# Optimization experiments

Hardware: AMD Instinct MI355X
Metric: run time of the kernel (lower is better)

## Reference

```python
import jax, jax.numpy as jnp
import numpy as np

N, P, D, C = 2048, 64, 512, 32   # bs*n_vars, patch_num, hidden_dim, cluster_num
H, DFF, L = 8, 2048, 3           # heads, ffn dim, encoder layers
TEMP = 10.0
EPS = 1e-10
LN_EPS = 1e-5


def setup_inputs() -> dict:
    key = jax.random.key(0)
    ks = jax.random.split(key, 18)
    s = 0.02  # small init to keep activations sane
    inp = {}
    inp["input_series"] = jax.random.normal(ks[0], (N, P, D), jnp.float32)
    pi = jax.random.uniform(ks[1], (C,), jnp.float32) + 0.1
    inp["text_pi"] = pi / pi.sum()
    A = jax.random.uniform(ks[2], (C, C), jnp.float32) + 0.1
    inp["text_A"] = A / A.sum(axis=1, keepdims=True)
    # stacked per-layer TransformerEncoderLayer params (torch post-norm, relu)
    inp["qkv_w"] = jax.random.normal(ks[3], (L, 3 * D, D), jnp.float32) * s
    inp["qkv_b"] = jnp.zeros((L, 3 * D), jnp.float32)
    inp["out_w"] = jax.random.normal(ks[4], (L, D, D), jnp.float32) * s
    inp["out_b"] = jnp.zeros((L, D), jnp.float32)
    inp["ln1_w"] = jnp.ones((L, D), jnp.float32)
    inp["ln1_b"] = jnp.zeros((L, D), jnp.float32)
    inp["ff1_w"] = jax.random.normal(ks[5], (L, DFF, D), jnp.float32) * s
    inp["ff1_b"] = jnp.zeros((L, DFF), jnp.float32)
    inp["ff2_w"] = jax.random.normal(ks[6], (L, D, DFF), jnp.float32) * s
    inp["ff2_b"] = jnp.zeros((L, D), jnp.float32)
    inp["ln2_w"] = jnp.ones((L, D), jnp.float32)
    inp["ln2_b"] = jnp.zeros((L, D), jnp.float32)
    inp["mus"] = jax.random.normal(ks[7], (C, D), jnp.float32)
    return inp


def _layer_norm(x, w, b):
    m = x.mean(axis=-1, keepdims=True)
    v = ((x - m) ** 2).mean(axis=-1, keepdims=True)
    return (x - m) * jax.lax.rsqrt(v + LN_EPS) * w + b


def _encoder_layer(x, qkv_w, qkv_b, out_w, out_b, ln1_w, ln1_b,
                   ff1_w, ff1_b, ff2_w, ff2_b, ln2_w, ln2_b):
    n, p, d = x.shape
    dh = d // H
    qkv = x @ qkv_w.T + qkv_b                       # [n,p,3d]
    q, k, v = jnp.split(qkv, 3, axis=-1)
    def split_heads(t):
        return t.reshape(n, p, H, dh).transpose(0, 2, 1, 3)  # [n,h,p,dh]
    q, k, v = split_heads(q), split_heads(k), split_heads(v)
    scores = jnp.einsum('nhqd,nhkd->nhqk', q, k) / (dh ** 0.5)
    attn = jax.nn.softmax(scores, axis=-1)
    o = jnp.einsum('nhqk,nhkd->nhqd', attn, v)
    o = o.transpose(0, 2, 1, 3).reshape(n, p, d)
    o = o @ out_w.T + out_b
    x = _layer_norm(x + o, ln1_w, ln1_b)            # post-norm
    f = jax.nn.relu(x @ ff1_w.T + ff1_b) @ ff2_w.T + ff2_b
    return _layer_norm(x + f, ln2_w, ln2_b)


def reference(input_series, text_pi, text_A, qkv_w, qkv_b, out_w, out_b,
              ln1_w, ln1_b, ff1_w, ff1_b, ff2_w, ff2_b, ln2_w, ln2_b, mus):
    x = input_series
    for l in range(L):
        x = _encoder_layer(x, qkv_w[l], qkv_b[l], out_w[l], out_b[l],
                           ln1_w[l], ln1_b[l], ff1_w[l], ff1_b[l],
                           ff2_w[l], ff2_b[l], ln2_w[l], ln2_b[l])
    emb_ts = x                                       # [N,P,D]
    # ClusterCenters: softmax of exp(-||x - tanh(mu)||^2 / T)
    mu = jnp.tanh(mus)                               # [C,D]
    dist = ((emb_ts ** 2).sum(-1)[..., None]
            + (mu ** 2).sum(-1)[None, None, :]
            - 2.0 * jnp.einsum('npd,cd->npc', emb_ts, mu))  # [N,P,C]
    z = jnp.exp(-dist / TEMP)
    logits_all = z / z.sum(axis=-1, keepdims=True)
    log_za = jnp.log(logits_all + EPS)               # [N,P,C]
    # sequential HMM-style recursion over patches
    l0 = jax.nn.softmax(jnp.log(text_pi + EPS)[None, :] + log_za[:, 0], axis=-1)
    def step(c, lz):
        c2 = jax.nn.softmax(jnp.log(c @ text_A + EPS) + lz, axis=-1)
        return c2, c2
    _, ys = jax.lax.scan(step, l0, jnp.swapaxes(log_za[:, 1:], 0, 1))  # [P-1,N,C]
    cluster_probs = jnp.concatenate([l0[:, None], jnp.swapaxes(ys, 0, 1)], axis=1)
    entropy_loss = -jnp.sum(cluster_probs * jnp.log(cluster_probs + EPS), axis=-1).mean()
    return (cluster_probs, emb_ts, text_pi, text_A, entropy_loss)
```

## Files before the change

kernel.cpp:

```cpp
#include <hip/hip_runtime.h>
#include <stdint.h>


typedef __bf16 bf16;
typedef __bf16 bf16x2 __attribute__((ext_vector_type(2)));
typedef __bf16 bf16x4 __attribute__((ext_vector_type(4)));
typedef __bf16 bf16x8 __attribute__((ext_vector_type(8)));
typedef float  f32x4  __attribute__((ext_vector_type(4)));
typedef float  f32x2  __attribute__((ext_vector_type(2)));

#define EPSF 1e-10f
#define NROWS 131072L

__device__ __forceinline__ float bflo(uint32_t u){ return __uint_as_float(u << 16); }
__device__ __forceinline__ float bfhi(uint32_t u){ return __uint_as_float(u & 0xffff0000u); }

__device__ __forceinline__ void gload_lds16(const bf16* g, bf16* l){
  __builtin_amdgcn_global_load_lds((const __attribute__((address_space(1))) uint32_t*)g,
                                   (__attribute__((address_space(3))) uint32_t*)l,
                                   16, 0, 0);
}

__global__ void k_f2bf(const float* __restrict__ in, bf16* __restrict__ out, long n){
  const long stride = (long)gridDim.x * blockDim.x * 4;
  for (long i = ((long)blockIdx.x * blockDim.x + threadIdx.x) * 4; i < n; i += stride){
    f32x4 v = *(const f32x4*)(in + i);
    bf16x4 o = { (bf16)v[0], (bf16)v[1], (bf16)v[2], (bf16)v[3] };
    *(bf16x4*)(out + i) = o;
  }
}


#define MFMA_PH(SM, SN)                                                       \
  {                                                                           \
    __builtin_amdgcn_s_setprio(1);                                            \
    _Pragma("unroll")                                                         \
    for (int kk = 0; kk < 2; kk++) {                                          \
      _Pragma("unroll")                                                       \
      for (int i2 = 0; i2 < 4; i2++) {                                        \
        _Pragma("unroll")                                                     \
        for (int j2 = 0; j2 < 2; j2++) {                                      \
          acc[(SM)*4+i2][(SN)*2+j2] = __builtin_amdgcn_mfma_f32_16x16x32_bf16(\
              a[i2][kk], b[SN][j2][kk], acc[(SM)*4+i2][(SN)*2+j2], 0, 0, 0);  \
        }                                                                     \
      }                                                                       \
    }                                                                         \
    __builtin_amdgcn_s_setprio(0);                                            \
  }

#define RD_A(SM)                                                              \
  _Pragma("unroll")                                                           \
  for (int i2 = 0; i2 < 4; i2++) {                                            \
    a[i2][0] = *(const bf16x8*)&Ac[(SM)*8192 + aBase + i2*1024 + sl0];        \
    a[i2][1] = *(const bf16x8*)&Ac[(SM)*8192 + aBase + i2*1024 + sl1];        \
  }

#define RD_B(SN)                                                              \
  _Pragma("unroll")                                                           \
  for (int j2 = 0; j2 < 2; j2++) {                                            \
    b[SN][j2][0] = *(const bf16x8*)&Bc[(SN)*8192 + bBase + j2*1024 + sl0];    \
    b[SN][j2][1] = *(const bf16x8*)&Bc[(SN)*8192 + bBase + j2*1024 + sl1];    \
  }

#define ISSUE_A(dst, RO, KK) \
  gload_lds16(gA + (long)(RO)*lda + (KK), (dst) + (RO)*64 + wsl)
#define ISSUE_B(dst, RO, KK) \
  gload_lds16(gB + (long)(RO)*K   + (KK), (dst) + (RO)*64 + wsl)

#define WAITV(N)  asm volatile("s_waitcnt vmcnt(" #N ")" ::: "memory")
#define WAITL0    asm volatile("s_waitcnt lgkmcnt(0)" ::: "memory")
#define BARRIER   { __builtin_amdgcn_s_barrier(); asm volatile("" ::: "memory"); }

template<int RELU>
__global__ __launch_bounds__(512, 2)
void gemm256(const bf16* __restrict__ A, long lda,
             const bf16* __restrict__ W,
             const float* __restrict__ bias,
             bf16* __restrict__ Cb, long K, int nbx)
{
  const int tid  = threadIdx.x;
  const int wid  = tid >> 6;
  const int lane = tid & 63;
  const int wr = wid >> 2, wc = wid & 3;
  const long ldc = (long)nbx * 256;

  const unsigned nwg = gridDim.x;
  const unsigned q   = nwg >> 3;
  const unsigned swz = (blockIdx.x & 7) * q + (blockIdx.x >> 3);
  const unsigned bx  = swz % (unsigned)nbx;
  const unsigned by  = swz / (unsigned)nbx;
  const long bm = (long)by * 256;
  const long bn = (long)bx * 256;

  __shared__ __align__(16) bf16 smem[65536];
  bf16* const As0 = smem;
  bf16* const Bs0 = smem + 16384;
  bf16* const As1 = smem + 32768;
  bf16* const Bs1 = smem + 49152;

  const int gswz = ((lane & 7) ^ ((lane >> 3) & 7)) * 8;
  const int wsl  = wid * 512;
  const bf16* gA = A + (bm + wid * 8 + (lane >> 3)) * lda + gswz;
  const bf16* gB = W + (bn + wid * 8 + (lane >> 3)) * K   + gswz;

  const int fr = lane & 15, fg = lane >> 4;
  const int aBase = (wr * 64 + fr) * 64;
  const int bBase = (wc * 32 + fr) * 64;
  const int sl0 = ((0 + fg) ^ (fr & 7)) * 8;
  const int sl1 = ((4 + fg) ^ (fr & 7)) * 8;

  f32x4 acc[8][4];
#pragma unroll
  for (int i = 0; i < 8; i++)
#pragma unroll
    for (int j = 0; j < 4; j++) acc[i][j] = (f32x4){0.f, 0.f, 0.f, 0.f};

  bf16x8 a[4][2];
  bf16x8 b[2][2][2];

  const int nt = (int)(K >> 6);

  ISSUE_A(As0, 0, 0);   ISSUE_A(As0, 64, 0);
  ISSUE_B(Bs0, 0, 0);   ISSUE_B(Bs0, 64, 0);
  ISSUE_A(As0, 128, 0); ISSUE_A(As0, 192, 0);
  ISSUE_B(Bs0, 128, 0); ISSUE_B(Bs0, 192, 0);
  ISSUE_A(As1, 0, 64);  ISSUE_A(As1, 64, 64);
  ISSUE_B(Bs1, 0, 64);  ISSUE_B(Bs1, 64, 64);
  WAITV(4);
  BARRIER;

  for (int t = 0; t < nt; t++){
    bf16* const Ac = (t & 1) ? As1 : As0;
    bf16* const Bc = (t & 1) ? Bs1 : Bs0;
    bf16* const An = (t & 1) ? As0 : As1;
    bf16* const Bn = (t & 1) ? Bs0 : Bs1;
    const bool s1 = (t + 1 < nt);
    const bool s2 = (t + 2 < nt);
    const long kn  = (long)(t + 1) << 6;
    const long kn2 = (long)(t + 2) << 6;

    RD_A(0); RD_B(0); RD_B(1);
    if (s1){ ISSUE_A(An, 128, kn); ISSUE_A(An, 192, kn); }
    WAITL0;
    MFMA_PH(0, 0);
    BARRIER;

    if (s1){ ISSUE_B(Bn, 128, kn); ISSUE_B(Bn, 192, kn); }
    MFMA_PH(0, 1);
    __builtin_amdgcn_sched_barrier(0);
    RD_A(1);
    BARRIER;

    if (s2){ ISSUE_A(Ac, 0, kn2); ISSUE_A(Ac, 64, kn2); }
    WAITL0;
    MFMA_PH(1, 0);
    BARRIER;

    if (s2){ ISSUE_B(Bc, 0, kn2); ISSUE_B(Bc, 64, kn2); }
    MFMA_PH(1, 1);
    if (s2){ WAITV(4); } else { WAITV(0); }
    BARRIER;
  }

  bf16* const cw = smem + wid * 1280;
  float bv[4];
#pragma unroll
  for (int sn = 0; sn < 2; sn++)
#pragma unroll
    for (int j2 = 0; j2 < 2; j2++)
      bv[sn * 2 + j2] = bias[bn + sn * 128 + wc * 32 + j2 * 16 + fr];

#pragma unroll
  for (int sm = 0; sm < 2; sm++){
#pragma unroll
    for (int sn = 0; sn < 2; sn++){
#pragma unroll
      for (int ch = 0; ch < 2; ch++){
#pragma unroll
        for (int i2 = 0; i2 < 2; i2++){
#pragma unroll
          for (int j2 = 0; j2 < 2; j2++){
#pragma unroll
            for (int r = 0; r < 4; r++){
              float v = acc[sm * 4 + ch * 2 + i2][sn * 2 + j2][r] + bv[sn * 2 + j2];
              if (RELU) v = fmaxf(v, 0.f);
              cw[(i2 * 16 + fg * 4 + r) * 40 + j2 * 16 + fr] = (bf16)v;
            }
          }
        }
        WAITL0;
        const long r0 = bm + sm * 128 + wr * 64 + ch * 32;
        const long c0 = bn + sn * 128 + wc * 32;
#pragma unroll
        for (int p = 0; p < 2; p++){
          const int row = p * 16 + (lane >> 2);
          const int colg = (lane & 3) * 8;
          bf16x8 o = *(const bf16x8*)&cw[row * 40 + colg];
          *(bf16x8*)&Cb[(r0 + row) * ldc + c0 + colg] = o;
        }
        WAITL0;
      }
    }
  }
}

__global__ __launch_bounds__(256)
void attention(bf16* __restrict__ qkv)
{
  const int blk = blockIdx.x;
  const long n = blk >> 3;
  const int h  = blk & 7;
  const int tid = threadIdx.x;
  const int wid = tid >> 6, lane = tid & 63;

  __shared__ __align__(16) bf16 Qs[64][72];
  __shared__ __align__(16) bf16 Ks[64][72];
  __shared__ __align__(16) bf16 Vt[64][72];

  bf16* base = qkv + n * 64 * 1536 + h * 64;

  for (int c = tid; c < 512; c += 256){
    const int row = c >> 3, col = (c & 7) * 8;
    const long go = (long)row * 1536 + col;
    *(bf16x8*)&Qs[row][col] = *(const bf16x8*)(base + go);
    *(bf16x8*)&Ks[row][col] = *(const bf16x8*)(base + 512 + go);
    bf16x8 v = *(const bf16x8*)(base + 1024 + go);
#pragma unroll
    for (int e = 0; e < 8; e++) Vt[col + e][row] = v[e];
  }
  __syncthreads();

  const int fr = lane & 15, fg = lane >> 4;
  f32x4 sacc[4];
#pragma unroll
  for (int j = 0; j < 4; j++) sacc[j] = (f32x4){0.f, 0.f, 0.f, 0.f};
#pragma unroll
  for (int ks = 0; ks < 2; ks++){
    bf16x8 aa = *(const bf16x8*)&Qs[wid * 16 + fr][ks * 32 + fg * 8];
#pragma unroll
    for (int j = 0; j < 4; j++){
      bf16x8 bb = *(const bf16x8*)&Ks[j * 16 + fr][ks * 32 + fg * 8];
      sacc[j] = __builtin_amdgcn_mfma_f32_16x16x32_bf16(aa, bb, sacc[j], 0, 0, 0);
    }
  }

  float pv[4][4];
#pragma unroll
  for (int r = 0; r < 4; r++){
    float m = -1e30f;
#pragma unroll
    for (int j = 0; j < 4; j++) m = fmaxf(m, sacc[j][r]);
#pragma unroll
    for (int msk = 1; msk < 16; msk <<= 1) m = fmaxf(m, __shfl_xor(m, msk));
    float s = 0.f;
#pragma unroll
    for (int j = 0; j < 4; j++){
      float p = __expf((sacc[j][r] - m) * 0.125f);
      pv[j][r] = p; s += p;
    }
#pragma unroll
    for (int msk = 1; msk < 16; msk <<= 1) s += __shfl_xor(s, msk);
    const float inv = 1.f / s;
#pragma unroll
    for (int j = 0; j < 4; j++) pv[j][r] *= inv;
  }

#pragma unroll
  for (int j = 0; j < 4; j++)
#pragma unroll
    for (int r = 0; r < 4; r++)
      Qs[wid * 16 + fg * 4 + r][j * 16 + fr] = (bf16)pv[j][r];
  __syncthreads();

  f32x4 oacc[4];
#pragma unroll
  for (int j = 0; j < 4; j++) oacc[j] = (f32x4){0.f, 0.f, 0.f, 0.f};
#pragma unroll
  for (int ks = 0; ks < 2; ks++){
    bf16x8 aa = *(const bf16x8*)&Qs[wid * 16 + fr][ks * 32 + fg * 8];
#pragma unroll
    for (int j = 0; j < 4; j++){
      bf16x8 bb = *(const bf16x8*)&Vt[j * 16 + fr][ks * 32 + fg * 8];
      oacc[j] = __builtin_amdgcn_mfma_f32_16x16x32_bf16(aa, bb, oacc[j], 0, 0, 0);
    }
  }
#pragma unroll
  for (int j = 0; j < 4; j++)
#pragma unroll
    for (int r = 0; r < 4; r++)
      base[(long)(wid * 16 + fg * 4 + r) * 1536 + j * 16 + fr] = (bf16)oacc[j][r];
}

__global__ __launch_bounds__(256)
void resid_ln(const bf16* __restrict__ X, const bf16* __restrict__ O,
              const float* __restrict__ w, const float* __restrict__ b,
              bf16* __restrict__ Y, float* __restrict__ EF)
{
  const int wid = threadIdx.x >> 6, lane = threadIdx.x & 63;
  const long row = (long)blockIdx.x * 4 + wid;
  const uint4 xu = ((const uint4*)(X + row * 512))[lane];
  const uint4 ou = ((const uint4*)(O + row * 512))[lane];
  float s[8];
  s[0] = bflo(xu.x) + bflo(ou.x);  s[1] = bfhi(xu.x) + bfhi(ou.x);
  s[2] = bflo(xu.y) + bflo(ou.y);  s[3] = bfhi(xu.y) + bfhi(ou.y);
  s[4] = bflo(xu.z) + bflo(ou.z);  s[5] = bfhi(xu.z) + bfhi(ou.z);
  s[6] = bflo(xu.w) + bflo(ou.w);  s[7] = bfhi(xu.w) + bfhi(ou.w);
  float sum = 0.f, sq = 0.f;
#pragma unroll
  for (int e = 0; e < 8; e++){ sum += s[e]; sq += s[e] * s[e]; }
#pragma unroll
  for (int m = 1; m < 64; m <<= 1){ sum += __shfl_xor(sum, m); sq += __shfl_xor(sq, m); }
  const float mean = sum * (1.f / 512.f);
  const float var  = sq * (1.f / 512.f) - mean * mean;
  const float rs   = rsqrtf(var + 1e-5f);
  const f32x4 w0 = *(const f32x4*)(w + 8 * lane);
  const f32x4 w1 = *(const f32x4*)(w + 8 * lane + 4);
  const f32x4 b0 = *(const f32x4*)(b + 8 * lane);
  const f32x4 b1 = *(const f32x4*)(b + 8 * lane + 4);
  float o[8];
#pragma unroll
  for (int e = 0; e < 4; e++) o[e]     = (s[e]     - mean) * rs * w0[e] + b0[e];
#pragma unroll
  for (int e = 0; e < 4; e++) o[e + 4] = (s[e + 4] - mean) * rs * w1[e] + b1[e];
  bf16x8 ov = { (bf16)o[0], (bf16)o[1], (bf16)o[2], (bf16)o[3],
                (bf16)o[4], (bf16)o[5], (bf16)o[6], (bf16)o[7] };
  *(bf16x8*)(Y + row * 512 + 8 * lane) = ov;
  if (EF){
    f32x4 e0 = { o[0], o[1], o[2], o[3] };
    f32x4 e1 = { o[4], o[5], o[6], o[7] };
    *(f32x4*)(EF + row * 512 + 8 * lane) = e0;
    *(f32x4*)(EF + row * 512 + 8 * lane + 4) = e1;
  }
}

__global__ __launch_bounds__(256)
void k_mu(const float* __restrict__ mus, bf16* __restrict__ mubf, float* __restrict__ munorm)
{
  const int c = blockIdx.x, tid = threadIdx.x, lane = tid & 63, wid = tid >> 6;
  const f32x2 v = *(const f32x2*)(mus + c * 512 + 2 * tid);
  const float t0 = tanhf(v[0]), t1 = tanhf(v[1]);
  bf16x2 o2 = { (bf16)t0, (bf16)t1 };
  *(bf16x2*)(mubf + c * 512 + 2 * tid) = o2;
  float sq = t0 * t0 + t1 * t1;
#pragma unroll
  for (int m = 1; m < 64; m <<= 1) sq += __shfl_xor(sq, m);
  __shared__ float red[4];
  if (lane == 0) red[wid] = sq;
  __syncthreads();
  if (tid == 0) munorm[c] = red[0] + red[1] + red[2] + red[3];
}

__global__ __launch_bounds__(256)
void cluster_logza(const bf16* __restrict__ X, const bf16* __restrict__ MU,
                   const float* __restrict__ munorm, float* __restrict__ out)
{
  const int tid = threadIdx.x, lane = tid & 63, wid = tid >> 6;
  __shared__ __align__(16) bf16 mus[32][512];
  __shared__ float xs[512];
  __shared__ float red[4];
  __shared__ float dots[32];
  for (int c = tid; c < 2048; c += 256){
    const int r = c >> 6, col = (c & 63) * 8;
    *(bf16x8*)&mus[r][col] = *(const bf16x8*)(MU + r * 512 + col);
  }
  const int cc = tid >> 3, seg = tid & 7;
  const long row0 = (long)blockIdx.x * 16;
  __syncthreads();
  for (int rr = 0; rr < 16; rr++){
    const long row = row0 + rr;
    const uint32_t u = ((const uint32_t*)(X + row * 512))[tid];
    const float aa = bflo(u), bb = bfhi(u);
    xs[2 * tid] = aa; xs[2 * tid + 1] = bb;
    float sq = aa * aa + bb * bb;
#pragma unroll
    for (int m = 1; m < 64; m <<= 1) sq += __shfl_xor(sq, m);
    if (lane == 0) red[wid] = sq;
    __syncthreads();
    const float xn = red[0] + red[1] + red[2] + red[3];
    float p = 0.f;
#pragma unroll
    for (int jj = 0; jj < 8; jj++){
      const int col = jj * 64 + seg * 8;
      bf16x8 m8 = *(const bf16x8*)&mus[cc][col];
      const float* xv = &xs[col];
#pragma unroll
      for (int e = 0; e < 8; e++) p += xv[e] * (float)m8[e];
    }
#pragma unroll
    for (int m = 1; m < 8; m <<= 1) p += __shfl_xor(p, m);
    if (seg == 0) dots[cc] = p;
    __syncthreads();
    if (tid < 32){
      const float dist = xn + munorm[tid] - 2.f * dots[tid];
      const float lg = -dist * 0.1f;
      float mx = lg;
#pragma unroll
      for (int m = 1; m < 32; m <<= 1) mx = fmaxf(mx, __shfl_xor(mx, m, 32));
      const float z = __expf(lg - mx);
      float s = z;
#pragma unroll
      for (int m = 1; m < 32; m <<= 1) s += __shfl_xor(s, m, 32);
      out[row * 32 + tid] = logf(z / s + EPSF);
    }
    __syncthreads();
  }
}

__global__ __launch_bounds__(256)
void k_hmm(const float* __restrict__ lza, const float* __restrict__ pi,
           const float* __restrict__ A, float* __restrict__ cp, float* __restrict__ ent)
{
  __shared__ float As[32][33];
  const int tid = threadIdx.x;
  for (int i = tid; i < 1024; i += 256) As[i >> 5][i & 31] = A[i];
  __syncthreads();
  const int j = tid & 31;
  const long n = (long)blockIdx.x * 8 + (tid >> 5);
  const float* lz = lza + n * 2048;

  float c = logf(pi[j] + EPSF) + lz[j];
  {
    float mx = c;
#pragma unroll
    for (int m = 1; m < 32; m <<= 1) mx = fmaxf(mx, __shfl_xor(mx, m, 32));
    float z = __expf(c - mx), s = z;
#pragma unroll
    for (int m = 1; m < 32; m <<= 1) s += __shfl_xor(s, m, 32);
    c = z / s;
  }
  cp[n * 2048 + j] = c;
  float ea = -c * logf(c + EPSF);

  for (int p = 1; p < 64; p++){
    float y = 0.f;
#pragma unroll
    for (int i = 0; i < 32; i++) y += __shfl(c, i, 32) * As[i][j];
    float t = logf(y + EPSF) + lz[p * 32 + j];
    float mx = t;
#pragma unroll
    for (int m = 1; m < 32; m <<= 1) mx = fmaxf(mx, __shfl_xor(mx, m, 32));
    float z = __expf(t - mx), s = z;
#pragma unroll
    for (int m = 1; m < 32; m <<= 1) s += __shfl_xor(s, m, 32);
    c = z / s;
    cp[n * 2048 + p * 32 + j] = c;
    ea += -c * logf(c + EPSF);
  }
#pragma unroll
  for (int m = 1; m < 32; m <<= 1) ea += __shfl_xor(ea, m, 32);
  if (j == 0) atomicAdd(ent, ea * (1.f / 131072.f));
}

extern "C" void kernel_launch(void* const* d_in, const int* in_sizes, int n_in,
                              void* d_out, int out_size, void* d_ws, size_t ws_size,
                              hipStream_t stream)
{
  (void)in_sizes; (void)n_in; (void)out_size; (void)ws_size;
  const float* in_series = (const float*)d_in[0];
  const float* pi    = (const float*)d_in[1];
  const float* Amat  = (const float*)d_in[2];
  const float* qkv_w = (const float*)d_in[3];
  const float* qkv_b = (const float*)d_in[4];
  const float* out_w = (const float*)d_in[5];
  const float* out_b = (const float*)d_in[6];
  const float* ln1_w = (const float*)d_in[7];
  const float* ln1_b = (const float*)d_in[8];
  const float* ff1_w = (const float*)d_in[9];
  const float* ff1_b = (const float*)d_in[10];
  const float* ff2_w = (const float*)d_in[11];
  const float* ff2_b = (const float*)d_in[12];
  const float* ln2_w = (const float*)d_in[13];
  const float* ln2_b = (const float*)d_in[14];
  const float* mus   = (const float*)d_in[15];

  char* ws = (char*)d_ws;
  bf16* region0 = (bf16*)(ws);
  bf16* xb      = (bf16*)(ws + 536870912L);
  bf16* oproj   = (bf16*)(ws + 671088640L);
  bf16* w_qkv   = (bf16*)(ws + 805306368L);
  bf16* w_out   = (bf16*)(ws + 810024960L);
  bf16* w_ff1   = (bf16*)(ws + 811597824L);
  bf16* w_ff2   = (bf16*)(ws + 817889280L);
  bf16* mubf    = (bf16*)(ws + 824180736L);
  float* munorm = (float*)(ws + 824213504L);
  float* logza  = (float*)(ws);

  float* out_f = (float*)d_out;
  float* cp    = out_f;
  float* emb   = out_f + 4194304L;
  float* o_pi  = out_f + 71303168L;
  float* o_A   = out_f + 71303200L;
  float* o_ent = out_f + 71304224L;

  k_f2bf<<<8192, 256, 0, stream>>>(in_series, xb, 67108864L);
  k_f2bf<<<1024, 256, 0, stream>>>(qkv_w, w_qkv, 2359296L);
  k_f2bf<<<1024, 256, 0, stream>>>(out_w, w_out, 786432L);
  k_f2bf<<<1024, 256, 0, stream>>>(ff1_w, w_ff1, 3145728L);
  k_f2bf<<<1024, 256, 0, stream>>>(ff2_w, w_ff2, 3145728L);
  k_mu<<<32, 256, 0, stream>>>(mus, mubf, munorm);

  for (int l = 0; l < 3; l++){
    gemm256<0><<<3072, 512, 0, stream>>>(xb, 512, w_qkv + (long)l * 786432L,
                                         qkv_b + (long)l * 1536, region0, 512, 6);
    attention<<<16384, 256, 0, stream>>>(region0);
    gemm256<0><<<1024, 512, 0, stream>>>(region0, 1536, w_out + (long)l * 262144L,
                                         out_b + (long)l * 512, oproj, 512, 2);
    resid_ln<<<32768, 256, 0, stream>>>(xb, oproj, ln1_w + (long)l * 512,
                                        ln1_b + (long)l * 512, xb, nullptr);
    gemm256<1><<<4096, 512, 0, stream>>>(xb, 512, w_ff1 + (long)l * 1048576L,
                                         ff1_b + (long)l * 2048, region0, 512, 8);
    gemm256<0><<<1024, 512, 0, stream>>>(region0, 2048, w_ff2 + (long)l * 1048576L,
                                         ff2_b + (long)l * 512, oproj, 2048, 2);
    resid_ln<<<32768, 256, 0, stream>>>(xb, oproj, ln2_w + (long)l * 512,
                                        ln2_b + (long)l * 512, xb,
                                        (l == 2) ? emb : nullptr);
  }

  cluster_logza<<<8192, 256, 0, stream>>>(xb, mubf, munorm, logza);
  hipMemsetAsync(o_ent, 0, 4, stream);
  k_hmm<<<256, 256, 0, stream>>>(logza, pi, Amat, cp, o_ent);
  hipMemcpyAsync(o_pi, pi, 32 * sizeof(float), hipMemcpyDeviceToDevice, stream);
  hipMemcpyAsync(o_A, Amat, 1024 * sizeof(float), hipMemcpyDeviceToDevice, stream);
}
```

Before: 3.973 ms.

## Restructure GEMM main loop with double-buffered register fragments and one-tile prefetch

Reworks the bf16 GEMM k-loop so A fragments are held in two register sets. The next tile's first quadrant is read from LDS while the current tile's MFMAs run. Global-to-LDS prefetch shrinks from two tiles ahead to one, and the loop uses partial lgkmcnt waits and extra barriers, aiming to overlap LDS reads with MFMA work. In exchange it raises register pressure and shortens the global-load lookahead, which could expose memory latency.

```diff
diff --git a/kernel.cpp b/kernel.cpp
--- a/kernel.cpp
+++ b/kernel.cpp
@@ -41,25 +41,25 @@
         _Pragma("unroll")                                                     \
         for (int j2 = 0; j2 < 2; j2++) {                                      \
           acc[(SM)*4+i2][(SN)*2+j2] = __builtin_amdgcn_mfma_f32_16x16x32_bf16(\
-              a[i2][kk], b[SN][j2][kk], acc[(SM)*4+i2][(SN)*2+j2], 0, 0, 0);  \
+              a[SM][i2][kk], b[SN][j2][kk], acc[(SM)*4+i2][(SN)*2+j2], 0,0,0);\
         }                                                                     \
       }                                                                       \
     }                                                                         \
     __builtin_amdgcn_s_setprio(0);                                            \
   }
 
-#define RD_A(SM)                                                              \
+#define RD_A2(BUF, DST, SRC)                                                  \
   _Pragma("unroll")                                                           \
   for (int i2 = 0; i2 < 4; i2++) {                                            \
-    a[i2][0] = *(const bf16x8*)&Ac[(SM)*8192 + aBase + i2*1024 + sl0];        \
-    a[i2][1] = *(const bf16x8*)&Ac[(SM)*8192 + aBase + i2*1024 + sl1];        \
-  }
-
-#define RD_B(SN)                                                              \
+    a[DST][i2][0] = *(const bf16x8*)&(BUF)[(SRC)*8192 + aBase + i2*1024 + sl0];\
+    a[DST][i2][1] = *(const bf16x8*)&(BUF)[(SRC)*8192 + aBase + i2*1024 + sl1];\
+  }
+
+#define RD_B2(BUF, DST, SRC)                                                  \
   _Pragma("unroll")                                                           \
   for (int j2 = 0; j2 < 2; j2++) {                                            \
-    b[SN][j2][0] = *(const bf16x8*)&Bc[(SN)*8192 + bBase + j2*1024 + sl0];    \
-    b[SN][j2][1] = *(const bf16x8*)&Bc[(SN)*8192 + bBase + j2*1024 + sl1];    \
+    b[DST][j2][0] = *(const bf16x8*)&(BUF)[(SRC)*8192 + bBase + j2*1024 + sl0];\
+    b[DST][j2][1] = *(const bf16x8*)&(BUF)[(SRC)*8192 + bBase + j2*1024 + sl1];\
   }
 
 #define ISSUE_A(dst, RO, KK) \
@@ -68,6 +68,7 @@
   gload_lds16(gB + (long)(RO)*K   + (KK), (dst) + (RO)*64 + wsl)
 
 #define WAITV(N)  asm volatile("s_waitcnt vmcnt(" #N ")" ::: "memory")
+#define LGKM(N)   asm volatile("s_waitcnt lgkmcnt(" #N ")" ::: "memory")
 #define WAITL0    asm volatile("s_waitcnt lgkmcnt(0)" ::: "memory")
 #define BARRIER   { __builtin_amdgcn_s_barrier(); asm volatile("" ::: "memory"); }
 
@@ -115,7 +116,7 @@
 #pragma unroll
     for (int j = 0; j < 4; j++) acc[i][j] = (f32x4){0.f, 0.f, 0.f, 0.f};
 
-  bf16x8 a[4][2];
+  bf16x8 a[2][4][2];
   bf16x8 b[2][2][2];
 
   const int nt = (int)(K >> 6);
@@ -124,10 +125,10 @@
   ISSUE_B(Bs0, 0, 0);   ISSUE_B(Bs0, 64, 0);
   ISSUE_A(As0, 128, 0); ISSUE_A(As0, 192, 0);
   ISSUE_B(Bs0, 128, 0); ISSUE_B(Bs0, 192, 0);
-  ISSUE_A(As1, 0, 64);  ISSUE_A(As1, 64, 64);
-  ISSUE_B(Bs1, 0, 64);  ISSUE_B(Bs1, 64, 64);
-  WAITV(4);
+  WAITV(2);
   BARRIER;
+  RD_A2(As0, 0, 0);
+  RD_B2(Bs0, 0, 0);
 
   for (int t = 0; t < nt; t++){
     bf16* const Ac = (t & 1) ? As1 : As0;
@@ -135,30 +136,36 @@
     bf16* const An = (t & 1) ? As0 : As1;
     bf16* const Bn = (t & 1) ? Bs0 : Bs1;
     const bool s1 = (t + 1 < nt);
-    const bool s2 = (t + 2 < nt);
-    const long kn  = (long)(t + 1) << 6;
-    const long kn2 = (long)(t + 2) << 6;
-
-    RD_A(0); RD_B(0); RD_B(1);
+    const long kn = (long)(t + 1) << 6;
+
+    RD_A2(Ac, 1, 1);
+    if (s1){ ISSUE_A(An, 0, kn); ISSUE_A(An, 64, kn); }
+    BARRIER;
+    LGKM(8);
+    MFMA_PH(0, 0);
+    if (s1){ WAITV(2); } else { WAITV(0); }
+    BARRIER;
+
+    RD_B2(Bc, 1, 1);
+    if (s1){ ISSUE_B(Bn, 0, kn); ISSUE_B(Bn, 64, kn); }
+    BARRIER;
+    LGKM(4);
+    MFMA_PH(1, 0);
+    if (s1){ WAITV(2); }
+    BARRIER;
+
     if (s1){ ISSUE_A(An, 128, kn); ISSUE_A(An, 192, kn); }
-    WAITL0;
-    MFMA_PH(0, 0);
+    BARRIER;
+    LGKM(0);
+    MFMA_PH(0, 1);
+    if (s1){ RD_A2(An, 0, 0); }
+    if (s1){ WAITV(2); }
     BARRIER;
 
     if (s1){ ISSUE_B(Bn, 128, kn); ISSUE_B(Bn, 192, kn); }
-    MFMA_PH(0, 1);
-    __builtin_amdgcn_sched_barrier(0);
-    RD_A(1);
-    BARRIER;
-
-    if (s2){ ISSUE_A(Ac, 0, kn2); ISSUE_A(Ac, 64, kn2); }
-    WAITL0;
-    MFMA_PH(1, 0);
-    BARRIER;
-
-    if (s2){ ISSUE_B(Bc, 0, kn2); ISSUE_B(Bc, 64, kn2); }
     MFMA_PH(1, 1);
-    if (s2){ WAITV(4); } else { WAITV(0); }
+    if (s1){ RD_B2(Bn, 0, 0); }
+    if (s1){ WAITV(2); }
     BARRIER;
   }
 
```

Result: slower. 4.258 ms (+7.2%).
